# Kernel tuning notes

Measured on AMD Instinct MI355X. Metric: run time of the kernel, lower is better.

## Reference

```python
import jax, jax.numpy as jnp
import numpy as np

NUM_HEADS = 12


def setup_inputs() -> dict:
    key = jax.random.key(0)
    ks = jax.random.split(key, 5)
    B, N, D = 8, 1024, 768
    x = jax.random.normal(ks[0], (B, N, D), dtype=jnp.float32)
    w_qkv = jax.random.normal(ks[1], (D, 3 * D), dtype=jnp.float32) * (D ** -0.5)
    b_qkv = jax.random.normal(ks[2], (3 * D,), dtype=jnp.float32) * 0.02
    w_proj = jax.random.normal(ks[3], (D, D), dtype=jnp.float32) * (D ** -0.5)
    b_proj = jax.random.normal(ks[4], (D,), dtype=jnp.float32) * 0.02
    return {"x": x, "w_qkv": w_qkv, "b_qkv": b_qkv, "w_proj": w_proj, "b_proj": b_proj}


def reference(x, w_qkv, b_qkv, w_proj, b_proj):
    B, N, D = x.shape
    H = NUM_HEADS
    hd = D // H
    scale = hd ** -0.5
    qkv = x @ w_qkv + b_qkv                      # [B, N, 3D]
    qkv = qkv.reshape(B, N, 3, H, hd)
    q, k, v = jnp.moveaxis(qkv, 2, 0)            # each [B, N, H, hd]
    # scores: [B, H, N, N]
    scores = jnp.einsum("bqhd,bkhd->bhqk", q, k) * scale
    attn = jax.nn.softmax(scores, axis=-1)
    a = jnp.einsum("bhqk,bkhd->bqhd", attn, v)   # [B, N, H, hd]
    a = a.reshape(B, N, D)
    return a @ w_proj + b_proj
```

## Files before the change

### kernel.cpp

```cpp
#include <hip/hip_runtime.h>

#define B_ 8
#define N_ 1024
#define D_ 768
#define H_ 12
#define HD 64
#define M_ (B_*N_)

typedef short short8 __attribute__((ext_vector_type(8)));
typedef float f32x4 __attribute__((ext_vector_type(4)));
typedef float f32x16 __attribute__((ext_vector_type(16)));
typedef int int4v __attribute__((ext_vector_type(4)));

__device__ __forceinline__ unsigned short f2bf(float f) {
    union { float f; unsigned int u; } c; c.f = f;
    unsigned int u = c.u;
    unsigned int r = (u + 0x7fffu + ((u >> 16) & 1u)) >> 16;
    return (unsigned short)r;
}

__device__ __forceinline__ float exp2_hw(float x) {
    float r;
    asm("v_exp_f32 %0, %1" : "=v"(r) : "v"(x));
    return r;
}

__device__ __forceinline__ unsigned int cvtpk_bf16(float a, float b) {
    unsigned int r;
    asm("v_cvt_pk_bf16_f32 %0, %1, %2" : "=v"(r) : "v"(a), "v"(b));
    return r;
}

#define PLSWAP(a, b) asm volatile("v_permlane32_swap_b32 %0, %1" : "+&v"(a), "+&v"(b))

__device__ __forceinline__ short8 pack4(unsigned int a, unsigned int b,
                                        unsigned int c, unsigned int d) {
    union { int4v i; short8 s; } u;
    u.i = (int4v){(int)a, (int)b, (int)c, (int)d};
    return u.s;
}

__device__ __forceinline__ void gload16(const void* g, void* l) {
    __builtin_amdgcn_global_load_lds(
        (const __attribute__((address_space(1))) unsigned int*)g,
        (__attribute__((address_space(3))) unsigned int*)l, 16, 0, 0);
}


__global__ __launch_bounds__(256) void prep_kernel(
    const float* __restrict__ x, const float* __restrict__ wqkv,
    const float* __restrict__ wproj,
    unsigned short* __restrict__ xb, unsigned short* __restrict__ wqkvT,
    unsigned short* __restrict__ wprojT)
{
    int bid = blockIdx.x, tid = threadIdx.x;
    if (bid < 6144) {
        int i = bid * 256 + tid;
        float4 v = reinterpret_cast<const float4*>(x)[i];
        ushort4 o;
        o.x = f2bf(v.x); o.y = f2bf(v.y); o.z = f2bf(v.z); o.w = f2bf(v.w);
        reinterpret_cast<ushort4*>(xb)[i] = o;
    } else if (bid < 6144 + 6912) {
        int i = (bid - 6144) * 256 + tid;
        int r = i / 2304, c = i - r * 2304;
        wqkvT[c * 768 + r] = f2bf(wqkv[i]);
    } else {
        int i = (bid - 13056) * 256 + tid;
        int r = i / 768, c = i - r * 768;
        wprojT[c * 768 + r] = f2bf(wproj[i]);
    }
}


template<int MODE>
__global__ __launch_bounds__(256) void gemm_kernel(
    const unsigned short* __restrict__ A,
    const unsigned short* __restrict__ Bt,
    const float* __restrict__ bias,
    float* __restrict__ outf,
    unsigned short* __restrict__ qo,
    unsigned short* __restrict__ ko,
    unsigned short* __restrict__ vo,
    int Ndim, int K)
{
    __shared__ alignas(16) unsigned short As[4096];
    __shared__ alignas(16) unsigned short Bs[4096];

    int tid = threadIdx.x;
    int lane = tid & 63, w = tid >> 6;
    int wr = w >> 1, wc = w & 1;

    int nbx = Ndim >> 7;
    int nwg = gridDim.x;
    int cpx = nwg >> 3;
    int sbid = (blockIdx.x & 7) * cpx + (blockIdx.x >> 3);
    int bx = sbid % nbx, by = sbid / nbx;
    int m0 = by * 128, n0 = bx * 128;

    int lr = lane & 15, lk8 = (lane >> 4) * 8;
    int org = (lane >> 4) * 4;

    int srow = tid >> 2;
    int selem = (tid & 3) * 8;
    const unsigned short* gA = A + (size_t)(m0 + srow) * K + selem;
    const unsigned short* gB = Bt + (size_t)(n0 + srow) * K + selem;
    unsigned short* lA = As + w * 512;
    unsigned short* lB = Bs + w * 512;

    f32x4 acc[4][4] = {};

    int KT = K >> 5;
    for (int kt = 0; kt < KT; ++kt) {
        int k0 = kt * 32;
        __syncthreads();
        gload16(gA + k0, lA);
        gload16(gA + (size_t)64 * K + k0, lA + 2048);
        gload16(gB + k0, lB);
        gload16(gB + (size_t)64 * K + k0, lB + 2048);
        __syncthreads();
        short8 af[4], bf[4];
        #pragma unroll
        for (int mi = 0; mi < 4; mi++)
            af[mi] = *reinterpret_cast<const short8*>(&As[(wr * 64 + mi * 16 + lr) * 32 + lk8]);
        #pragma unroll
        for (int ni = 0; ni < 4; ni++)
            bf[ni] = *reinterpret_cast<const short8*>(&Bs[(wc * 64 + ni * 16 + lr) * 32 + lk8]);
        #pragma unroll
        for (int mi = 0; mi < 4; mi++)
            #pragma unroll
            for (int ni = 0; ni < 4; ni++)
                acc[mi][ni] = (MODE == 1)
                    ? __builtin_amdgcn_mfma_f32_16x16x32_bf16(bf[ni], af[mi], acc[mi][ni], 0, 0, 0)
                    : __builtin_amdgcn_mfma_f32_16x16x32_bf16(af[mi], bf[ni], acc[mi][ni], 0, 0, 0);
    }

    if (MODE == 1) {
        int m = m0 + wr * 64 + lr;
        #pragma unroll
        for (int mi = 0; mi < 4; mi++) {
            int row = m + mi * 16;
            #pragma unroll
            for (int ni = 0; ni < 4; ni++) {
                int col = n0 + wc * 64 + ni * 16 + org;
                float4 bv = *reinterpret_cast<const float4*>(&bias[col]);
                float4 o;
                o.x = acc[mi][ni][0] + bv.x;
                o.y = acc[mi][ni][1] + bv.y;
                o.z = acc[mi][ni][2] + bv.z;
                o.w = acc[mi][ni][3] + bv.w;
                *reinterpret_cast<float4*>(&outf[(size_t)row * Ndim + col]) = o;
            }
        }
        return;
    }

    if (n0 >= 1536) {
        #pragma unroll
        for (int mi = 0; mi < 4; mi++) {
            int nn0g = m0 + wr * 64 + mi * 16 + org;
            int b = nn0g >> 10, nn = nn0g & 1023;
            #pragma unroll
            for (int ni = 0; ni < 4; ni++) {
                int colg = n0 + wc * 64 + ni * 16 + lr;
                int rem = colg - 1536;
                int h = rem >> 6, dd = rem & 63;
                float bv = bias[colg];
                unsigned long long u = 0;
                #pragma unroll
                for (int r = 0; r < 4; r++)
                    u |= (unsigned long long)f2bf(acc[mi][ni][r] + bv) << (16 * r);
                *reinterpret_cast<unsigned long long*>(
                    vo + ((size_t)(b * H_ + h) * HD + dd) * N_ + nn) = u;
            }
        }
    } else {
        int which = n0 / 768;
        unsigned short* dst = (which == 0) ? qo : ko;
        float fold = (which == 0) ? 0.125f * 1.44269504088896f : 1.0f;
        #pragma unroll
        for (int mi = 0; mi < 4; mi++) {
            #pragma unroll
            for (int ni = 0; ni < 4; ni++) {
                int col = n0 + wc * 64 + ni * 16 + lr;
                int rem = col - which * 768;
                int h = rem >> 6, dd = rem & 63;
                float bv = bias[col];
                #pragma unroll
                for (int r = 0; r < 4; r++) {
                    int row = m0 + wr * 64 + mi * 16 + org + r;
                    int b = row >> 10, nn = row & 1023;
                    dst[(((size_t)(b * H_ + h) * N_ + nn) * HD) + dd] =
                        f2bf((acc[mi][ni][r] + bv) * fold);
                }
            }
        }
    }
}


__global__ __launch_bounds__(256) void attn_kernel(
    const unsigned short* __restrict__ qg,
    const unsigned short* __restrict__ kg,
    const unsigned short* __restrict__ vtg,
    unsigned short* __restrict__ aout)
{
    __shared__ alignas(16) unsigned short Ks[2][4096];
    __shared__ alignas(16) unsigned short Vs[2][4096];

    int tid = threadIdx.x;
    int lane = tid & 63, w = tid >> 6;

    int bid = blockIdx.x;
    int xcd = bid & 7;
    int chunk = bid >> 3;
    int bh = xcd * 12 + (chunk % 12);
    int qblk = chunk / 12;
    int b = bh / H_, h = bh - b * H_;
    int q0w = qblk * 128 + w * 32;
    int l31 = lane & 31;
    int hi = lane >> 5;
    int swz = l31 & 7;

    const unsigned short* qp = qg + ((size_t)bh * N_ + q0w + l31) * HD + hi * 8;
    short8 qf[4];
    #pragma unroll
    for (int ds = 0; ds < 4; ds++)
        qf[ds] = *reinterpret_cast<const short8*>(qp + ds * 16);

    const unsigned short* kbh = kg + (size_t)bh * N_ * HD;
    const unsigned short* vtbh = vtg + (size_t)bh * HD * N_;

    int sr0 = tid >> 3;
    int sj0 = (tid & 7) ^ (sr0 & 7);
    int sr1 = sr0 + 32;
    int sj1 = (tid & 7) ^ (sr1 & 7);

    float m_run = -INFINITY, l_run = 0.f;
    f32x16 o0 = {}, o1 = {};

#define STAGE(buf, kv0)                                                        \
    do {                                                                       \
        gload16(kbh + (size_t)((kv0) + sr0) * HD + sj0 * 8, &Ks[buf][w * 512]);\
        gload16(kbh + (size_t)((kv0) + sr1) * HD + sj1 * 8, &Ks[buf][2048 + w * 512]);\
        gload16(vtbh + (size_t)sr0 * N_ + (kv0) + sj0 * 8, &Vs[buf][w * 512]); \
        gload16(vtbh + (size_t)sr1 * N_ + (kv0) + sj1 * 8, &Vs[buf][2048 + w * 512]);\
    } while (0)

    STAGE(0, 0);
    asm volatile("s_waitcnt vmcnt(0)" ::: "memory");
    __builtin_amdgcn_s_barrier();
    __builtin_amdgcn_sched_barrier(0);

    int cur = 0;
    for (int t = 0; t < 16; ++t) {
        if (t < 15) STAGE(cur ^ 1, (t + 1) * 64);

        const unsigned short* Ksb = Ks[cur];
        const unsigned short* Vsb = Vs[cur];

        f32x16 s0 = {}, s1 = {};
        #pragma unroll
        for (int ds = 0; ds < 4; ds++) {
            int pc = (ds * 2 + hi) ^ swz;
            short8 kf0 = *reinterpret_cast<const short8*>(&Ksb[(l31) * 64 + pc * 8]);
            short8 kf1 = *reinterpret_cast<const short8*>(&Ksb[(32 + l31) * 64 + pc * 8]);
            s0 = __builtin_amdgcn_mfma_f32_32x32x16_bf16(kf0, qf[ds], s0, 0, 0, 0);
            s1 = __builtin_amdgcn_mfma_f32_32x32x16_bf16(kf1, qf[ds], s1, 0, 0, 0);
        }

        float mx = s0[0];
        #pragma unroll
        for (int r = 1; r < 16; r++) mx = fmaxf(mx, s0[r]);
        #pragma unroll
        for (int r = 0; r < 16; r++) mx = fmaxf(mx, s1[r]);
        mx = fmaxf(mx, __shfl_xor(mx, 32, 64));

        if (__any(mx > m_run + 8.f)) {
            float mn = fmaxf(m_run, mx);
            float al = exp2_hw(m_run - mn);
            m_run = mn;
            l_run *= al;
            o0 *= al;
            o1 *= al;
        }

        float psum = 0.f;
        #pragma unroll
        for (int r = 0; r < 16; r++) { float p = exp2_hw(s0[r] - m_run); psum += p; s0[r] = p; }
        #pragma unroll
        for (int r = 0; r < 16; r++) { float p = exp2_hw(s1[r] - m_run); psum += p; s1[r] = p; }

        l_run += psum + __shfl_xor(psum, 32, 64);

        unsigned int c0[8], c1[8];
        #pragma unroll
        for (int i = 0; i < 8; i++) c0[i] = cvtpk_bf16(s0[2 * i], s0[2 * i + 1]);
        #pragma unroll
        for (int i = 0; i < 8; i++) c1[i] = cvtpk_bf16(s1[2 * i], s1[2 * i + 1]);
        PLSWAP(c0[0], c0[2]); PLSWAP(c0[1], c0[3]);
        PLSWAP(c0[4], c0[6]); PLSWAP(c0[5], c0[7]);
        PLSWAP(c1[0], c1[2]); PLSWAP(c1[1], c1[3]);
        PLSWAP(c1[4], c1[6]); PLSWAP(c1[5], c1[7]);
        short8 pa0 = pack4(c0[0], c0[1], c0[2], c0[3]);
        short8 pa1 = pack4(c0[4], c0[5], c0[6], c0[7]);
        short8 pa2 = pack4(c1[0], c1[1], c1[2], c1[3]);
        short8 pa3 = pack4(c1[4], c1[5], c1[6], c1[7]);

        #pragma unroll
        for (int ks = 0; ks < 4; ks++) {
            int pc = (ks * 2 + hi) ^ swz;
            short8 vf0 = *reinterpret_cast<const short8*>(&Vsb[(l31) * 64 + pc * 8]);
            short8 vf1 = *reinterpret_cast<const short8*>(&Vsb[(32 + l31) * 64 + pc * 8]);
            short8 pa = (ks == 0) ? pa0 : (ks == 1) ? pa1 : (ks == 2) ? pa2 : pa3;
            o0 = __builtin_amdgcn_mfma_f32_32x32x16_bf16(vf0, pa, o0, 0, 0, 0);
            o1 = __builtin_amdgcn_mfma_f32_32x32x16_bf16(vf1, pa, o1, 0, 0, 0);
        }

        if (t < 15) {
            asm volatile("s_waitcnt vmcnt(0)" ::: "memory");
            __builtin_amdgcn_s_barrier();
            __builtin_amdgcn_sched_barrier(0);
            cur ^= 1;
        }
    }
#undef STAGE

    float linv = 1.0f / l_run;
    unsigned short* op = aout + ((size_t)(b * N_ + q0w + l31)) * D_ + h * HD;
    #pragma unroll
    for (int rg = 0; rg < 4; rg++) {
        int dbase = 8 * rg + 4 * hi;
        unsigned long long u0 = 0, u1 = 0;
        #pragma unroll
        for (int k = 0; k < 4; k++) {
            u0 |= (unsigned long long)f2bf(o0[rg * 4 + k] * linv) << (16 * k);
            u1 |= (unsigned long long)f2bf(o1[rg * 4 + k] * linv) << (16 * k);
        }
        *reinterpret_cast<unsigned long long*>(op + dbase) = u0;
        *reinterpret_cast<unsigned long long*>(op + 32 + dbase) = u1;
    }
}


extern "C" void kernel_launch(void* const* d_in, const int* in_sizes, int n_in,
                              void* d_out, int out_size, void* d_ws, size_t ws_size,
                              hipStream_t stream) {
    const float* x      = (const float*)d_in[0];
    const float* w_qkv  = (const float*)d_in[1];
    const float* b_qkv  = (const float*)d_in[2];
    const float* w_proj = (const float*)d_in[3];
    const float* b_proj = (const float*)d_in[4];
    float* out = (float*)d_out;

    char* ws = (char*)d_ws;
    unsigned short* xb     = (unsigned short*)(ws + 0);
    unsigned short* wqkvT  = (unsigned short*)(ws + 12582912);
    unsigned short* wprojT = (unsigned short*)(ws + 16121856);
    unsigned short* qb     = (unsigned short*)(ws + 17301504);
    unsigned short* kb     = (unsigned short*)(ws + 29884416);
    unsigned short* vtb    = (unsigned short*)(ws + 42467328);
    unsigned short* aout   = xb;

    prep_kernel<<<15360, 256, 0, stream>>>(x, w_qkv, w_proj, xb, wqkvT, wprojT);

    gemm_kernel<0><<<1152, 256, 0, stream>>>(
        xb, wqkvT, b_qkv, nullptr, qb, kb, vtb, 3 * D_, D_);

    attn_kernel<<<768, 256, 0, stream>>>(qb, kb, vtb, aout);

    gemm_kernel<1><<<384, 256, 0, stream>>>(
        aout, wprojT, b_proj, out, nullptr, nullptr, nullptr, D_, D_);
}
```

Baseline: 148.6 us.

## Double-buffer GEMM LDS tiles and switch to a 2D grid without block swizzle

The GEMM kernel now keeps two LDS buffers and prefetches the next K-tile through direct global-to-LDS loads while MFMAs run on the current tile. This cuts the loop from two barriers per iteration to one, so load latency can overlap with compute. The launch also moves to a 2D grid and drops the XCD-aware block remapping, which may change L2 locality across chiplets. LDS use doubles, which could lower occupancy.

```diff
diff --git a/kernel.cpp b/kernel.cpp
--- a/kernel.cpp
+++ b/kernel.cpp
@@ -83,19 +83,14 @@
     unsigned short* __restrict__ vo,
     int Ndim, int K)
 {
-    __shared__ alignas(16) unsigned short As[4096];
-    __shared__ alignas(16) unsigned short Bs[4096];
+    __shared__ alignas(16) unsigned short As[2][4096];
+    __shared__ alignas(16) unsigned short Bs[2][4096];
 
     int tid = threadIdx.x;
     int lane = tid & 63, w = tid >> 6;
     int wr = w >> 1, wc = w & 1;
 
-    int nbx = Ndim >> 7;
-    int nwg = gridDim.x;
-    int cpx = nwg >> 3;
-    int sbid = (blockIdx.x & 7) * cpx + (blockIdx.x >> 3);
-    int bx = sbid % nbx, by = sbid / nbx;
-    int m0 = by * 128, n0 = bx * 128;
+    int m0 = blockIdx.y * 128, n0 = blockIdx.x * 128;
 
     int lr = lane & 15, lk8 = (lane >> 4) * 8;
     int org = (lane >> 4) * 4;
@@ -104,27 +99,34 @@
     int selem = (tid & 3) * 8;
     const unsigned short* gA = A + (size_t)(m0 + srow) * K + selem;
     const unsigned short* gB = Bt + (size_t)(n0 + srow) * K + selem;
-    unsigned short* lA = As + w * 512;
-    unsigned short* lB = Bs + w * 512;
 
     f32x4 acc[4][4] = {};
 
+#define GSTAGE(buf, k0)                                                    \
+    do {                                                                   \
+        gload16(gA + (k0), &As[buf][w * 512]);                             \
+        gload16(gA + (size_t)64 * K + (k0), &As[buf][2048 + w * 512]);     \
+        gload16(gB + (k0), &Bs[buf][w * 512]);                             \
+        gload16(gB + (size_t)64 * K + (k0), &Bs[buf][2048 + w * 512]);     \
+    } while (0)
+
+    GSTAGE(0, 0);
+    asm volatile("s_waitcnt vmcnt(0)" ::: "memory");
+    __builtin_amdgcn_s_barrier();
+    __builtin_amdgcn_sched_barrier(0);
+
     int KT = K >> 5;
+    int cur = 0;
     for (int kt = 0; kt < KT; ++kt) {
-        int k0 = kt * 32;
-        __syncthreads();
-        gload16(gA + k0, lA);
-        gload16(gA + (size_t)64 * K + k0, lA + 2048);
-        gload16(gB + k0, lB);
-        gload16(gB + (size_t)64 * K + k0, lB + 2048);
-        __syncthreads();
+        if (kt + 1 < KT) GSTAGE(cur ^ 1, (kt + 1) * 32);
+
         short8 af[4], bf[4];
         #pragma unroll
         for (int mi = 0; mi < 4; mi++)
-            af[mi] = *reinterpret_cast<const short8*>(&As[(wr * 64 + mi * 16 + lr) * 32 + lk8]);
+            af[mi] = *reinterpret_cast<const short8*>(&As[cur][(wr * 64 + mi * 16 + lr) * 32 + lk8]);
         #pragma unroll
         for (int ni = 0; ni < 4; ni++)
-            bf[ni] = *reinterpret_cast<const short8*>(&Bs[(wc * 64 + ni * 16 + lr) * 32 + lk8]);
+            bf[ni] = *reinterpret_cast<const short8*>(&Bs[cur][(wc * 64 + ni * 16 + lr) * 32 + lk8]);
         #pragma unroll
         for (int mi = 0; mi < 4; mi++)
             #pragma unroll
@@ -132,7 +134,15 @@
                 acc[mi][ni] = (MODE == 1)
                     ? __builtin_amdgcn_mfma_f32_16x16x32_bf16(bf[ni], af[mi], acc[mi][ni], 0, 0, 0)
                     : __builtin_amdgcn_mfma_f32_16x16x32_bf16(af[mi], bf[ni], acc[mi][ni], 0, 0, 0);
-    }
+
+        if (kt + 1 < KT) {
+            asm volatile("s_waitcnt vmcnt(0)" ::: "memory");
+            __builtin_amdgcn_s_barrier();
+            __builtin_amdgcn_sched_barrier(0);
+            cur ^= 1;
+        }
+    }
+#undef GSTAGE
 
     if (MODE == 1) {
         int m = m0 + wr * 64 + lr;
@@ -363,11 +373,11 @@
 
     prep_kernel<<<15360, 256, 0, stream>>>(x, w_qkv, w_proj, xb, wqkvT, wprojT);
 
-    gemm_kernel<0><<<1152, 256, 0, stream>>>(
+    gemm_kernel<0><<<dim3(18, 64), 256, 0, stream>>>(
         xb, wqkvT, b_qkv, nullptr, qb, kb, vtb, 3 * D_, D_);
 
     attn_kernel<<<768, 256, 0, stream>>>(qb, kb, vtb, aout);
 
-    gemm_kernel<1><<<384, 256, 0, stream>>>(
+    gemm_kernel<1><<<dim3(6, 64), 256, 0, stream>>>(
         aout, wprojT, b_proj, out, nullptr, nullptr, nullptr, D_, D_);
 }
```

After: 146.8 us. About the same (-1.2%).
